# Kernel optimization log

Measured on AMD Instinct MI355X. Metric: run time of the kernel, lower is better.

Reference implementation:

```python
import jax, jax.numpy as jnp
import numpy as np

EPS = 1e-5
AVG_D_LOG = 2.302585092994046  # avg_d['log'] = log(10)

N, D, F, FE = 65536, 16, 64, 16
POST_IN = (4 * 3 + 1) * F  # (n_agg*n_scalers + 1) * in_dim = 832


def setup_inputs() -> dict:
    key = jax.random.key(0)
    ks = jax.random.split(key, 8)
    h = jax.random.normal(ks[0], (N, F), dtype=jnp.float32)
    edge_attr = jax.random.normal(ks[1], (N, D, FE), dtype=jnp.float32)
    nbr_idx = jax.random.randint(ks[2], (N, D), 0, N)
    pre_in = 2 * F + FE
    W_pre = jax.random.normal(ks[3], (pre_in, F), dtype=jnp.float32) / np.sqrt(pre_in)
    b_pre = jnp.zeros((F,), dtype=jnp.float32)
    W_post1 = jax.random.normal(ks[4], (POST_IN, F), dtype=jnp.float32) / np.sqrt(POST_IN)
    b_post1 = jnp.zeros((F,), dtype=jnp.float32)
    W_post2 = jax.random.normal(ks[5], (F, F), dtype=jnp.float32) / np.sqrt(F)
    b_post2 = jnp.zeros((F,), dtype=jnp.float32)
    return {"h": h, "edge_attr": edge_attr, "nbr_idx": nbr_idx,
            "W_pre": W_pre, "b_pre": b_pre,
            "W_post1": W_post1, "b_post1": b_post1,
            "W_post2": W_post2, "b_post2": b_post2}


def reference(h, edge_attr, nbr_idx, W_pre, b_pre, W_post1, b_post1, W_post2, b_post2):
    # pretrans: message MLP on cat([src_feat, dst_feat, edge_attr])
    h_src = h[nbr_idx]                                   # [N, D, F]
    h_dst = jnp.broadcast_to(h[:, None, :], h_src.shape)  # [N, D, F]
    z = jnp.concatenate([h_src, h_dst, edge_attr], axis=-1)  # [N, D, 2F+FE]
    e = jax.nn.relu(jnp.einsum('ndi,io->ndo', z, W_pre) + b_pre)  # [N, D, F]

    # multi-aggregator neighbor reduction (dim=-2)
    mean = jnp.mean(e, axis=-2)
    mx = jnp.max(e, axis=-2)
    mn = jnp.min(e, axis=-2)
    var = jax.nn.relu(jnp.mean(e * e, axis=-2) - mean * mean)
    std = jnp.sqrt(var + EPS)
    agg = jnp.concatenate([mean, mx, mn, std], axis=-1)  # [N, 4F]

    # degree scalers (fixed in-degree D)
    logD = jnp.asarray(np.log(D + 1.0), dtype=h.dtype)
    amp = agg * (logD / AVG_D_LOG)
    att = agg * (AVG_D_LOG / logD)
    agg = jnp.concatenate([agg, amp, att], axis=-1)      # [N, 12F]

    # posttrans MLP on cat([h, aggregated]) with residual (in_dim == out_dim)
    x = jnp.concatenate([h, agg], axis=-1)               # [N, 13F]
    x = jax.nn.relu(x @ W_post1 + b_post1)
    x = x @ W_post2 + b_post2
    return x + h
```

## Files before the change

kernel.cpp:

```cpp
#include <hip/hip_runtime.h>
#include <hip/hip_bf16.h>
#include <math.h>


#define N_NODES 65536
#define NBLK (N_NODES / 16)
#define GRID_PREP (NBLK + 64)
#define ASTRIDE 348
#define YSTRIDE 76

typedef float f32x4 __attribute__((ext_vector_type(4)));
typedef float f32x16 __attribute__((ext_vector_type(16)));
typedef short s16x8 __attribute__((ext_vector_type(8)));
typedef unsigned short us4 __attribute__((ext_vector_type(4)));
typedef int i32x4 __attribute__((ext_vector_type(4)));

__device__ __forceinline__ unsigned short f2bf(float f) {
    union { float f; unsigned int u; } v; v.f = f;
    unsigned int r = v.u + 0x7fffu + ((v.u >> 16) & 1u);
    return (unsigned short)(r >> 16);
}
__device__ __forceinline__ unsigned short f2bfh(float f) {
    __hip_bfloat16 b = __float2bfloat16(f);
    union { __hip_bfloat16 b; unsigned short u; } v; v.b = b; return v.u;
}
__device__ __forceinline__ float bf2f(unsigned short u) {
    union { unsigned int u; float f; } v; v.u = ((unsigned int)u) << 16; return v.f;
}

__global__ __launch_bounds__(256) void k_prep(const float* __restrict__ h,
                                              const float* __restrict__ Wpre,
                                              const float* __restrict__ b_pre,
                                              const float* __restrict__ Wp1,
                                              const float* __restrict__ Wp2,
                                              unsigned short* __restrict__ u,
                                              unsigned short* __restrict__ vbf,
                                              unsigned short* __restrict__ wfullT,
                                              unsigned short* __restrict__ w3T,
                                              unsigned short* __restrict__ wp2T,
                                              float c1, float c2) {
    int t = threadIdx.x;
    if (blockIdx.x >= NBLK) {
        int c = blockIdx.x - NBLK;
        for (int k = t; k < 320; k += 256) {
            float v;
            if (k < 64) v = Wp1[k * 64 + c];
            else {
                int kk = k - 64;
                v = Wp1[(64 + kk) * 64 + c] + c1 * Wp1[(320 + kk) * 64 + c]
                                            + c2 * Wp1[(576 + kk) * 64 + c];
            }
            wfullT[c * 320 + k] = f2bf(v);
        }
        if (t < 16)              w3T[c * 16 + t]         = f2bf(Wpre[(128 + t) * 64 + c]);
        if (t >= 64 && t < 128)  wp2T[c * 64 + (t - 64)] = f2bf(Wp2[(t - 64) * 64 + c]);
        return;
    }

    __shared__ unsigned short hl[16 * 68];
    int lane = t & 63;
    int wv = __builtin_amdgcn_readfirstlane(t) >> 6;
    int c = lane & 15, g = lane >> 4;
    int node0 = blockIdx.x * 16;
    {
        int r = t >> 4, q = t & 15;
        float4 hv = *((const float4*)(h + (size_t)node0 * 64) + t);
        us4 o;
        o.x = f2bfh(hv.x); o.y = f2bfh(hv.y); o.z = f2bfh(hv.z); o.w = f2bfh(hv.w);
        *(us4*)&hl[r * 68 + q * 4] = o;
    }
    s16x8 bf[2][2];
    int woff = (wv < 2) ? 0 : 64;
    #pragma unroll
    for (int i2 = 0; i2 < 2; ++i2) {
        int wcol = ((wv & 1) * 32) + i2 * 16 + c;
        #pragma unroll
        for (int ks = 0; ks < 2; ++ks) {
            #pragma unroll
            for (int j = 0; j < 8; ++j)
                bf[i2][ks][j] = (short)f2bfh(Wpre[(woff + ks * 32 + g * 8 + j) * 64 + wcol]);
        }
    }
    __syncthreads();
    f32x4 acc0 = {0.f, 0.f, 0.f, 0.f}, acc1 = {0.f, 0.f, 0.f, 0.f};
    #pragma unroll
    for (int ks = 0; ks < 2; ++ks) {
        s16x8 a = *(const s16x8*)&hl[c * 68 + ks * 32 + g * 8];
        acc0 = __builtin_amdgcn_mfma_f32_16x16x32_bf16(a, bf[0][ks], acc0, 0, 0, 0);
        acc1 = __builtin_amdgcn_mfma_f32_16x16x32_bf16(a, bf[1][ks], acc1, 0, 0, 0);
    }
    unsigned short* dst = (wv < 2) ? u : vbf;
    #pragma unroll
    for (int i2 = 0; i2 < 2; ++i2) {
        int dcol = ((wv & 1) * 32) + i2 * 16 + c;
        float bp = (wv < 2) ? b_pre[dcol] : 0.f;
        const f32x4& av = i2 ? acc1 : acc0;
        #pragma unroll
        for (int i = 0; i < 4; ++i) {
            int row = g * 4 + i;
            dst[(size_t)(node0 + row) * 64 + dcol] = f2bfh(av[i] + bp);
        }
    }
}

__global__ __launch_bounds__(256, 4) void k_main(
    const float* __restrict__ h,
    const float* __restrict__ edge_attr,
    const int* __restrict__ nbr_idx,
    const float* __restrict__ b_post1,
    const float* __restrict__ b_post2,
    const unsigned short* __restrict__ u,
    const unsigned short* __restrict__ vbf,
    const unsigned short* __restrict__ wfullT,
    const unsigned short* __restrict__ w3T,
    const unsigned short* __restrict__ wp2T,
    float* __restrict__ out) {
    __shared__ unsigned short A_lds[16 * ASTRIDE];
    __shared__ unsigned short y1_lds[16 * YSTRIDE];
    __shared__ int nbl[256];

    int t = threadIdx.x;
    int lane = t & 63;
    int wu2 = __builtin_amdgcn_readfirstlane(t) >> 6;
    int c = lane & 15;
    int g = lane >> 4;
    int l32 = lane & 31;
    int h2 = lane >> 5;
    int ct = wu2 & 1;
    int wr = wu2 >> 1;
    int colb = ct * 32 + l32;
    int cb2 = colb * 2;
    int col16 = wu2 * 16 + c;
    int node0 = blockIdx.x * 16;

    s16x8 w3b = *(const s16x8*)&w3T[colb * 16 + h2 * 8];
    float b1c = b_post1[col16];
    float b2c = b_post2[col16];

    {
        int r = t >> 4, q = t & 15;
        float4 hv = *((const float4*)(h + (size_t)node0 * 64) + t);
        us4 o;
        o.x = f2bfh(hv.x); o.y = f2bfh(hv.y); o.z = f2bfh(hv.z); o.w = f2bfh(hv.w);
        *(us4*)&A_lds[r * ASTRIDE + q * 4] = o;
        nbl[t] = nbr_idx[node0 * 16 + t] << 7;
    }
    __syncthreads();

    const char* ub = (const char*)u;
    const char* vb = (const char*)vbf + ((unsigned)node0 << 7) + (unsigned)(wr * 256) + cb2;
    const char* eb = (const char*)edge_attr
                   + ((size_t)node0 * 16 + wr * 32 + l32) * 64 + h2 * 32;

    #pragma unroll
    for (int it = 0; it < 4; ++it) {
        int rt = wr + 2 * it;

        float4 x0 = *(const float4*)(eb + it * 4096);
        float4 x1 = *(const float4*)(eb + it * 4096 + 16);
        s16x8 a;
        a[0] = (short)f2bfh(x0.x); a[1] = (short)f2bfh(x0.y);
        a[2] = (short)f2bfh(x0.z); a[3] = (short)f2bfh(x0.w);
        a[4] = (short)f2bfh(x1.x); a[5] = (short)f2bfh(x1.y);
        a[6] = (short)f2bfh(x1.z); a[7] = (short)f2bfh(x1.w);

        f32x16 acc = {};
        acc = __builtin_amdgcn_mfma_f32_32x32x16_bf16(a, w3b, acc, 0, 0, 0);

        i32x4 jq0 = *(const i32x4*)&nbl[rt * 32 + 4 * h2 + 0];
        i32x4 jq1 = *(const i32x4*)&nbl[rt * 32 + 4 * h2 + 8];
        i32x4 jq2 = *(const i32x4*)&nbl[rt * 32 + 4 * h2 + 16];
        i32x4 jq3 = *(const i32x4*)&nbl[rt * 32 + 4 * h2 + 24];
        float uv[16];
        #pragma unroll
        for (int i = 0; i < 4; ++i) {
            uv[i]      = bf2f(*(const unsigned short*)(ub + (unsigned)(jq0[i] + cb2)));
            uv[4 + i]  = bf2f(*(const unsigned short*)(ub + (unsigned)(jq1[i] + cb2)));
            uv[8 + i]  = bf2f(*(const unsigned short*)(ub + (unsigned)(jq2[i] + cb2)));
            uv[12 + i] = bf2f(*(const unsigned short*)(ub + (unsigned)(jq3[i] + cb2)));
        }
        float v0 = bf2f(*(const unsigned short*)(vb + it * 512));
        float v1 = bf2f(*(const unsigned short*)(vb + it * 512 + 128));

        float e0  = fmaxf(acc[0]  + uv[0]  + v0, 0.f);
        float e1  = fmaxf(acc[1]  + uv[1]  + v0, 0.f);
        float e2  = fmaxf(acc[2]  + uv[2]  + v0, 0.f);
        float e3  = fmaxf(acc[3]  + uv[3]  + v0, 0.f);
        float e4  = fmaxf(acc[4]  + uv[4]  + v0, 0.f);
        float e5  = fmaxf(acc[5]  + uv[5]  + v0, 0.f);
        float e6  = fmaxf(acc[6]  + uv[6]  + v0, 0.f);
        float e7  = fmaxf(acc[7]  + uv[7]  + v0, 0.f);
        float e8  = fmaxf(acc[8]  + uv[8]  + v1, 0.f);
        float e9  = fmaxf(acc[9]  + uv[9]  + v1, 0.f);
        float e10 = fmaxf(acc[10] + uv[10] + v1, 0.f);
        float e11 = fmaxf(acc[11] + uv[11] + v1, 0.f);
        float e12 = fmaxf(acc[12] + uv[12] + v1, 0.f);
        float e13 = fmaxf(acc[13] + uv[13] + v1, 0.f);
        float e14 = fmaxf(acc[14] + uv[14] + v1, 0.f);
        float e15 = fmaxf(acc[15] + uv[15] + v1, 0.f);

        float s1a = ((e0 + e1) + (e2 + e3)) + ((e4 + e5) + (e6 + e7));
        float s2a = fmaf(e0, e0, fmaf(e1, e1, fmaf(e2, e2, e3 * e3)))
                  + fmaf(e4, e4, fmaf(e5, e5, fmaf(e6, e6, e7 * e7)));
        float mxa = fmaxf(fmaxf(fmaxf(fmaxf(fmaxf(fmaxf(fmaxf(e0, e1), e2), e3), e4), e5), e6), e7);
        float mna = fminf(fminf(fminf(fminf(fminf(fminf(fminf(e0, e1), e2), e3), e4), e5), e6), e7);
        float s1b = ((e8 + e9) + (e10 + e11)) + ((e12 + e13) + (e14 + e15));
        float s2b = fmaf(e8, e8, fmaf(e9, e9, fmaf(e10, e10, e11 * e11)))
                  + fmaf(e12, e12, fmaf(e13, e13, fmaf(e14, e14, e15 * e15)));
        float mxb = fmaxf(fmaxf(fmaxf(fmaxf(fmaxf(fmaxf(fmaxf(e8, e9), e10), e11), e12), e13), e14), e15);
        float mnb = fminf(fminf(fminf(fminf(fminf(fminf(fminf(e8, e9), e10), e11), e12), e13), e14), e15);

        s1a += __shfl_xor(s1a, 32); s2a += __shfl_xor(s2a, 32);
        mxa = fmaxf(mxa, __shfl_xor(mxa, 32)); mna = fminf(mna, __shfl_xor(mna, 32));
        s1b += __shfl_xor(s1b, 32); s2b += __shfl_xor(s2b, 32);
        mxb = fmaxf(mxb, __shfl_xor(mxb, 32)); mnb = fminf(mnb, __shfl_xor(mnb, 32));

        float ma = s1a * 0.0625f;
        float sda = sqrtf(fmaxf(fmaf(-ma, ma, s2a * 0.0625f), 0.f) + 1e-5f);
        float mb = s1b * 0.0625f;
        float sdb = sqrtf(fmaxf(fmaf(-mb, mb, s2b * 0.0625f), 0.f) + 1e-5f);

        if (h2 == 0) {
            unsigned short* pa = &A_lds[(2 * rt) * ASTRIDE + 64 + colb];
            pa[0]   = f2bfh(ma);
            pa[64]  = f2bfh(mxa);
            pa[128] = f2bfh(mna);
            pa[192] = f2bfh(sda);
            unsigned short* pb = &A_lds[(2 * rt + 1) * ASTRIDE + 64 + colb];
            pb[0]   = f2bfh(mb);
            pb[64]  = f2bfh(mxb);
            pb[128] = f2bfh(mnb);
            pb[192] = f2bfh(sdb);
        }
    }
    __syncthreads();

    {
        f32x4 y1 = {0.f, 0.f, 0.f, 0.f};
        #pragma unroll
        for (int ks = 0; ks < 10; ++ks) {
            s16x8 wf = *(const s16x8*)&wfullT[col16 * 320 + ks * 32 + g * 8];
            s16x8 a  = *(const s16x8*)&A_lds[c * ASTRIDE + ks * 32 + g * 8];
            y1 = __builtin_amdgcn_mfma_f32_16x16x32_bf16(a, wf, y1, 0, 0, 0);
        }
        #pragma unroll
        for (int i = 0; i < 4; ++i)
            y1_lds[(g * 4 + i) * YSTRIDE + col16] = f2bfh(fmaxf(y1[i] + b1c, 0.f));
    }
    __syncthreads();

    {
        f32x4 o = {0.f, 0.f, 0.f, 0.f};
        #pragma unroll
        for (int ks = 0; ks < 2; ++ks) {
            s16x8 wf = *(const s16x8*)&wp2T[col16 * 64 + ks * 32 + g * 8];
            s16x8 a  = *(const s16x8*)&y1_lds[c * YSTRIDE + ks * 32 + g * 8];
            o = __builtin_amdgcn_mfma_f32_16x16x32_bf16(a, wf, o, 0, 0, 0);
        }
        #pragma unroll
        for (int i = 0; i < 4; ++i) {
            int r = g * 4 + i;
            out[(size_t)(node0 + r) * 64 + col16] =
                o[i] + b2c + h[(size_t)(node0 + r) * 64 + col16];
        }
    }
}

extern "C" void kernel_launch(void* const* d_in, const int* in_sizes, int n_in,
                              void* d_out, int out_size, void* d_ws, size_t ws_size,
                              hipStream_t stream) {
    const float* h         = (const float*)d_in[0];
    const float* edge_attr = (const float*)d_in[1];
    const int*   nbr_idx   = (const int*)d_in[2];
    const float* W_pre     = (const float*)d_in[3];
    const float* b_pre     = (const float*)d_in[4];
    const float* W_post1   = (const float*)d_in[5];
    const float* b_post1   = (const float*)d_in[6];
    const float* W_post2   = (const float*)d_in[7];
    const float* b_post2   = (const float*)d_in[8];
    float* out = (float*)d_out;

    size_t need = (size_t)N_NODES * 64 * 2 * 2 + (64 * 320 + 64 * 16 + 64 * 64) * 2;
    if (ws_size < need) return;
    unsigned short* u      = (unsigned short*)d_ws;
    unsigned short* vbf    = u + (size_t)N_NODES * 64;
    unsigned short* wfullT = vbf + (size_t)N_NODES * 64;
    unsigned short* w3T    = wfullT + 64 * 320;
    unsigned short* wp2T   = w3T + 64 * 16;

    double ld = log(16.0 + 1.0);
    const double AVG = 2.302585092994046;
    float c1 = (float)(ld / AVG);
    float c2 = (float)(AVG / ld);

    k_prep<<<GRID_PREP, 256, 0, stream>>>(h, W_pre, b_pre, W_post1, W_post2,
                                          u, vbf, wfullT, w3T, wp2T, c1, c2);
    k_main<<<NBLK, 256, 0, stream>>>(h, edge_attr, nbr_idx, b_post1, b_post2,
                                     u, vbf, wfullT, w3T, wp2T, out);
}
```

Before: 64.31 us.

## Software-pipeline neighbor gathers and prefetch post-MLP weights before barriers

The neighbor-index LDS staging and its barrier are removed, and indices are read directly from global memory. The gather loop is restructured into ISSUE/COMPUTE stages so the loads for the next iteration are in flight while the current one computes. The reduction writes are split by half-wave so no lane sits idle. Weight fragments for both post-MLP matmuls are loaded into registers before the barriers so their latency hides behind synchronisation. In exchange, register pressure rises with two stages of gathered values live at once, which under the occupancy target of 4 may cause spills.

```diff
diff --git a/kernel.cpp b/kernel.cpp
--- a/kernel.cpp
+++ b/kernel.cpp
@@ -117,7 +117,6 @@
     float* __restrict__ out) {
     __shared__ unsigned short A_lds[16 * ASTRIDE];
     __shared__ unsigned short y1_lds[16 * YSTRIDE];
-    __shared__ int nbl[256];
 
     int t = threadIdx.x;
     int lane = t & 63;
@@ -137,125 +136,142 @@
     float b1c = b_post1[col16];
     float b2c = b_post2[col16];
 
+    const char* ub = (const char*)u;
+    const char* vb = (const char*)vbf + ((unsigned)node0 << 7) + (unsigned)(wr * 256) + cb2;
+    const char* eb = (const char*)edge_attr
+                   + ((size_t)node0 * 16 + wr * 32 + l32) * 64 + h2 * 32;
+
     {
         int r = t >> 4, q = t & 15;
         float4 hv = *((const float4*)(h + (size_t)node0 * 64) + t);
         us4 o;
         o.x = f2bfh(hv.x); o.y = f2bfh(hv.y); o.z = f2bfh(hv.z); o.w = f2bfh(hv.w);
         *(us4*)&A_lds[r * ASTRIDE + q * 4] = o;
-        nbl[t] = nbr_idx[node0 * 16 + t] << 7;
-    }
-    __syncthreads();
-
-    const char* ub = (const char*)u;
-    const char* vb = (const char*)vbf + ((unsigned)node0 << 7) + (unsigned)(wr * 256) + cb2;
-    const char* eb = (const char*)edge_attr
-                   + ((size_t)node0 * 16 + wr * 32 + l32) * 64 + h2 * 32;
-
+    }
+
+#define ISSUE(S, IT)                                                           \
+    const int* nb##S = nbr_idx + node0 * 16 + (wr + 2 * (IT)) * 32 + 4 * h2;   \
+    i32x4 ja##S = *(const i32x4*)(nb##S);                                      \
+    i32x4 jb##S = *(const i32x4*)(nb##S + 8);                                  \
+    i32x4 jc##S = *(const i32x4*)(nb##S + 16);                                 \
+    i32x4 jd##S = *(const i32x4*)(nb##S + 24);                                 \
+    float4 xa##S = *(const float4*)(eb + (IT) * 4096);                         \
+    float4 xb##S = *(const float4*)(eb + (IT) * 4096 + 16);                    \
+    unsigned short g0##S  = *(const unsigned short*)(ub + (unsigned)((ja##S[0] << 7) + cb2)); \
+    unsigned short g1##S  = *(const unsigned short*)(ub + (unsigned)((ja##S[1] << 7) + cb2)); \
+    unsigned short g2##S  = *(const unsigned short*)(ub + (unsigned)((ja##S[2] << 7) + cb2)); \
+    unsigned short g3##S  = *(const unsigned short*)(ub + (unsigned)((ja##S[3] << 7) + cb2)); \
+    unsigned short g4##S  = *(const unsigned short*)(ub + (unsigned)((jb##S[0] << 7) + cb2)); \
+    unsigned short g5##S  = *(const unsigned short*)(ub + (unsigned)((jb##S[1] << 7) + cb2)); \
+    unsigned short g6##S  = *(const unsigned short*)(ub + (unsigned)((jb##S[2] << 7) + cb2)); \
+    unsigned short g7##S  = *(const unsigned short*)(ub + (unsigned)((jb##S[3] << 7) + cb2)); \
+    unsigned short g8##S  = *(const unsigned short*)(ub + (unsigned)((jc##S[0] << 7) + cb2)); \
+    unsigned short g9##S  = *(const unsigned short*)(ub + (unsigned)((jc##S[1] << 7) + cb2)); \
+    unsigned short g10##S = *(const unsigned short*)(ub + (unsigned)((jc##S[2] << 7) + cb2)); \
+    unsigned short g11##S = *(const unsigned short*)(ub + (unsigned)((jc##S[3] << 7) + cb2)); \
+    unsigned short g12##S = *(const unsigned short*)(ub + (unsigned)((jd##S[0] << 7) + cb2)); \
+    unsigned short g13##S = *(const unsigned short*)(ub + (unsigned)((jd##S[1] << 7) + cb2)); \
+    unsigned short g14##S = *(const unsigned short*)(ub + (unsigned)((jd##S[2] << 7) + cb2)); \
+    unsigned short g15##S = *(const unsigned short*)(ub + (unsigned)((jd##S[3] << 7) + cb2)); \
+    unsigned short va##S = *(const unsigned short*)(vb + (IT) * 512);          \
+    unsigned short vc##S = *(const unsigned short*)(vb + (IT) * 512 + 128);
+
+#define COMPUTE(S, IT) {                                                       \
+    s16x8 a;                                                                   \
+    a[0] = (short)f2bfh(xa##S.x); a[1] = (short)f2bfh(xa##S.y);                \
+    a[2] = (short)f2bfh(xa##S.z); a[3] = (short)f2bfh(xa##S.w);                \
+    a[4] = (short)f2bfh(xb##S.x); a[5] = (short)f2bfh(xb##S.y);                \
+    a[6] = (short)f2bfh(xb##S.z); a[7] = (short)f2bfh(xb##S.w);                \
+    f32x16 acc = {};                                                           \
+    acc = __builtin_amdgcn_mfma_f32_32x32x16_bf16(a, w3b, acc, 0, 0, 0);       \
+    float v0 = bf2f(va##S), v1 = bf2f(vc##S);                                  \
+    float e0  = fmaxf(acc[0]  + bf2f(g0##S)  + v0, 0.f);                       \
+    float e1  = fmaxf(acc[1]  + bf2f(g1##S)  + v0, 0.f);                       \
+    float e2  = fmaxf(acc[2]  + bf2f(g2##S)  + v0, 0.f);                       \
+    float e3  = fmaxf(acc[3]  + bf2f(g3##S)  + v0, 0.f);                       \
+    float e4  = fmaxf(acc[4]  + bf2f(g4##S)  + v0, 0.f);                       \
+    float e5  = fmaxf(acc[5]  + bf2f(g5##S)  + v0, 0.f);                       \
+    float e6  = fmaxf(acc[6]  + bf2f(g6##S)  + v0, 0.f);                       \
+    float e7  = fmaxf(acc[7]  + bf2f(g7##S)  + v0, 0.f);                       \
+    float e8  = fmaxf(acc[8]  + bf2f(g8##S)  + v1, 0.f);                       \
+    float e9  = fmaxf(acc[9]  + bf2f(g9##S)  + v1, 0.f);                       \
+    float e10 = fmaxf(acc[10] + bf2f(g10##S) + v1, 0.f);                       \
+    float e11 = fmaxf(acc[11] + bf2f(g11##S) + v1, 0.f);                       \
+    float e12 = fmaxf(acc[12] + bf2f(g12##S) + v1, 0.f);                       \
+    float e13 = fmaxf(acc[13] + bf2f(g13##S) + v1, 0.f);                       \
+    float e14 = fmaxf(acc[14] + bf2f(g14##S) + v1, 0.f);                       \
+    float e15 = fmaxf(acc[15] + bf2f(g15##S) + v1, 0.f);                       \
+    float s1a = ((e0 + e1) + (e2 + e3)) + ((e4 + e5) + (e6 + e7));             \
+    float s2a = fmaf(e0, e0, fmaf(e1, e1, fmaf(e2, e2, e3 * e3)))              \
+              + fmaf(e4, e4, fmaf(e5, e5, fmaf(e6, e6, e7 * e7)));             \
+    float mxa = fmaxf(fmaxf(fmaxf(e0, e1), fmaxf(e2, e3)),                     \
+                      fmaxf(fmaxf(e4, e5), fmaxf(e6, e7)));                    \
+    float mna = fminf(fminf(fminf(e0, e1), fminf(e2, e3)),                     \
+                      fminf(fminf(e4, e5), fminf(e6, e7)));                    \
+    float s1b = ((e8 + e9) + (e10 + e11)) + ((e12 + e13) + (e14 + e15));       \
+    float s2b = fmaf(e8, e8, fmaf(e9, e9, fmaf(e10, e10, e11 * e11)))          \
+              + fmaf(e12, e12, fmaf(e13, e13, fmaf(e14, e14, e15 * e15)));     \
+    float mxb = fmaxf(fmaxf(fmaxf(e8, e9), fmaxf(e10, e11)),                   \
+                      fmaxf(fmaxf(e12, e13), fmaxf(e14, e15)));                \
+    float mnb = fminf(fminf(fminf(e8, e9), fminf(e10, e11)),                   \
+                      fminf(fminf(e12, e13), fminf(e14, e15)));                \
+    s1a += __shfl_xor(s1a, 32); s2a += __shfl_xor(s2a, 32);                    \
+    mxa = fmaxf(mxa, __shfl_xor(mxa, 32)); mna = fminf(mna, __shfl_xor(mna, 32)); \
+    s1b += __shfl_xor(s1b, 32); s2b += __shfl_xor(s2b, 32);                    \
+    mxb = fmaxf(mxb, __shfl_xor(mxb, 32)); mnb = fminf(mnb, __shfl_xor(mnb, 32)); \
+    float S1 = h2 ? s1b : s1a;                                                 \
+    float S2 = h2 ? s2b : s2a;                                                 \
+    float MX = h2 ? mxb : mxa;                                                 \
+    float MN = h2 ? mnb : mna;                                                 \
+    float M  = S1 * 0.0625f;                                                   \
+    float SD = sqrtf(fmaxf(fmaf(-M, M, S2 * 0.0625f), 0.f) + 1e-5f);           \
+    unsigned short* pd = &A_lds[(2 * (wr + 2 * (IT)) + h2) * ASTRIDE + 64 + colb]; \
+    pd[0]   = f2bfh(M);                                                        \
+    pd[64]  = f2bfh(MX);                                                       \
+    pd[128] = f2bfh(MN);                                                       \
+    pd[192] = f2bfh(SD);                                                       \
+}
+
+    ISSUE(T0, 0)
+    ISSUE(T1, 1)
+    COMPUTE(T0, 0)
+    ISSUE(T2, 2)
+    COMPUTE(T1, 1)
+    ISSUE(T3, 3)
+    COMPUTE(T2, 2)
+    COMPUTE(T3, 3)
+#undef ISSUE
+#undef COMPUTE
+
+    s16x8 wf[10];
     #pragma unroll
-    for (int it = 0; it < 4; ++it) {
-        int rt = wr + 2 * it;
-
-        float4 x0 = *(const float4*)(eb + it * 4096);
-        float4 x1 = *(const float4*)(eb + it * 4096 + 16);
-        s16x8 a;
-        a[0] = (short)f2bfh(x0.x); a[1] = (short)f2bfh(x0.y);
-        a[2] = (short)f2bfh(x0.z); a[3] = (short)f2bfh(x0.w);
-        a[4] = (short)f2bfh(x1.x); a[5] = (short)f2bfh(x1.y);
-        a[6] = (short)f2bfh(x1.z); a[7] = (short)f2bfh(x1.w);
-
-        f32x16 acc = {};
-        acc = __builtin_amdgcn_mfma_f32_32x32x16_bf16(a, w3b, acc, 0, 0, 0);
-
-        i32x4 jq0 = *(const i32x4*)&nbl[rt * 32 + 4 * h2 + 0];
-        i32x4 jq1 = *(const i32x4*)&nbl[rt * 32 + 4 * h2 + 8];
-        i32x4 jq2 = *(const i32x4*)&nbl[rt * 32 + 4 * h2 + 16];
-        i32x4 jq3 = *(const i32x4*)&nbl[rt * 32 + 4 * h2 + 24];
-        float uv[16];
-        #pragma unroll
-        for (int i = 0; i < 4; ++i) {
-            uv[i]      = bf2f(*(const unsigned short*)(ub + (unsigned)(jq0[i] + cb2)));
-            uv[4 + i]  = bf2f(*(const unsigned short*)(ub + (unsigned)(jq1[i] + cb2)));
-            uv[8 + i]  = bf2f(*(const unsigned short*)(ub + (unsigned)(jq2[i] + cb2)));
-            uv[12 + i] = bf2f(*(const unsigned short*)(ub + (unsigned)(jq3[i] + cb2)));
-        }
-        float v0 = bf2f(*(const unsigned short*)(vb + it * 512));
-        float v1 = bf2f(*(const unsigned short*)(vb + it * 512 + 128));
-
-        float e0  = fmaxf(acc[0]  + uv[0]  + v0, 0.f);
-        float e1  = fmaxf(acc[1]  + uv[1]  + v0, 0.f);
-        float e2  = fmaxf(acc[2]  + uv[2]  + v0, 0.f);
-        float e3  = fmaxf(acc[3]  + uv[3]  + v0, 0.f);
-        float e4  = fmaxf(acc[4]  + uv[4]  + v0, 0.f);
-        float e5  = fmaxf(acc[5]  + uv[5]  + v0, 0.f);
-        float e6  = fmaxf(acc[6]  + uv[6]  + v0, 0.f);
-        float e7  = fmaxf(acc[7]  + uv[7]  + v0, 0.f);
-        float e8  = fmaxf(acc[8]  + uv[8]  + v1, 0.f);
-        float e9  = fmaxf(acc[9]  + uv[9]  + v1, 0.f);
-        float e10 = fmaxf(acc[10] + uv[10] + v1, 0.f);
-        float e11 = fmaxf(acc[11] + uv[11] + v1, 0.f);
-        float e12 = fmaxf(acc[12] + uv[12] + v1, 0.f);
-        float e13 = fmaxf(acc[13] + uv[13] + v1, 0.f);
-        float e14 = fmaxf(acc[14] + uv[14] + v1, 0.f);
-        float e15 = fmaxf(acc[15] + uv[15] + v1, 0.f);
-
-        float s1a = ((e0 + e1) + (e2 + e3)) + ((e4 + e5) + (e6 + e7));
-        float s2a = fmaf(e0, e0, fmaf(e1, e1, fmaf(e2, e2, e3 * e3)))
-                  + fmaf(e4, e4, fmaf(e5, e5, fmaf(e6, e6, e7 * e7)));
-        float mxa = fmaxf(fmaxf(fmaxf(fmaxf(fmaxf(fmaxf(fmaxf(e0, e1), e2), e3), e4), e5), e6), e7);
-        float mna = fminf(fminf(fminf(fminf(fminf(fminf(fminf(e0, e1), e2), e3), e4), e5), e6), e7);
-        float s1b = ((e8 + e9) + (e10 + e11)) + ((e12 + e13) + (e14 + e15));
-        float s2b = fmaf(e8, e8, fmaf(e9, e9, fmaf(e10, e10, e11 * e11)))
-                  + fmaf(e12, e12, fmaf(e13, e13, fmaf(e14, e14, e15 * e15)));
-        float mxb = fmaxf(fmaxf(fmaxf(fmaxf(fmaxf(fmaxf(fmaxf(e8, e9), e10), e11), e12), e13), e14), e15);
-        float mnb = fminf(fminf(fminf(fminf(fminf(fminf(fminf(e8, e9), e10), e11), e12), e13), e14), e15);
-
-        s1a += __shfl_xor(s1a, 32); s2a += __shfl_xor(s2a, 32);
-        mxa = fmaxf(mxa, __shfl_xor(mxa, 32)); mna = fminf(mna, __shfl_xor(mna, 32));
-        s1b += __shfl_xor(s1b, 32); s2b += __shfl_xor(s2b, 32);
-        mxb = fmaxf(mxb, __shfl_xor(mxb, 32)); mnb = fminf(mnb, __shfl_xor(mnb, 32));
-
-        float ma = s1a * 0.0625f;
-        float sda = sqrtf(fmaxf(fmaf(-ma, ma, s2a * 0.0625f), 0.f) + 1e-5f);
-        float mb = s1b * 0.0625f;
-        float sdb = sqrtf(fmaxf(fmaf(-mb, mb, s2b * 0.0625f), 0.f) + 1e-5f);
-
-        if (h2 == 0) {
-            unsigned short* pa = &A_lds[(2 * rt) * ASTRIDE + 64 + colb];
-            pa[0]   = f2bfh(ma);
-            pa[64]  = f2bfh(mxa);
-            pa[128] = f2bfh(mna);
-            pa[192] = f2bfh(sda);
-            unsigned short* pb = &A_lds[(2 * rt + 1) * ASTRIDE + 64 + colb];
-            pb[0]   = f2bfh(mb);
-            pb[64]  = f2bfh(mxb);
-            pb[128] = f2bfh(mnb);
-            pb[192] = f2bfh(sdb);
-        }
-    }
+    for (int ks = 0; ks < 10; ++ks)
+        wf[ks] = *(const s16x8*)&wfullT[col16 * 320 + ks * 32 + g * 8];
     __syncthreads();
 
     {
         f32x4 y1 = {0.f, 0.f, 0.f, 0.f};
         #pragma unroll
         for (int ks = 0; ks < 10; ++ks) {
-            s16x8 wf = *(const s16x8*)&wfullT[col16 * 320 + ks * 32 + g * 8];
-            s16x8 a  = *(const s16x8*)&A_lds[c * ASTRIDE + ks * 32 + g * 8];
-            y1 = __builtin_amdgcn_mfma_f32_16x16x32_bf16(a, wf, y1, 0, 0, 0);
+            s16x8 a = *(const s16x8*)&A_lds[c * ASTRIDE + ks * 32 + g * 8];
+            y1 = __builtin_amdgcn_mfma_f32_16x16x32_bf16(a, wf[ks], y1, 0, 0, 0);
         }
         #pragma unroll
         for (int i = 0; i < 4; ++i)
             y1_lds[(g * 4 + i) * YSTRIDE + col16] = f2bfh(fmaxf(y1[i] + b1c, 0.f));
     }
+
+    s16x8 wp0 = *(const s16x8*)&wp2T[col16 * 64 + 0 * 32 + g * 8];
+    s16x8 wp1 = *(const s16x8*)&wp2T[col16 * 64 + 1 * 32 + g * 8];
     __syncthreads();
 
     {
         f32x4 o = {0.f, 0.f, 0.f, 0.f};
-        #pragma unroll
-        for (int ks = 0; ks < 2; ++ks) {
-            s16x8 wf = *(const s16x8*)&wp2T[col16 * 64 + ks * 32 + g * 8];
-            s16x8 a  = *(const s16x8*)&y1_lds[c * YSTRIDE + ks * 32 + g * 8];
-            o = __builtin_amdgcn_mfma_f32_16x16x32_bf16(a, wf, o, 0, 0, 0);
+        {
+            s16x8 a0 = *(const s16x8*)&y1_lds[c * YSTRIDE + 0 * 32 + g * 8];
+            s16x8 a1 = *(const s16x8*)&y1_lds[c * YSTRIDE + 1 * 32 + g * 8];
+            o = __builtin_amdgcn_mfma_f32_16x16x32_bf16(a0, wp0, o, 0, 0, 0);
+            o = __builtin_amdgcn_mfma_f32_16x16x32_bf16(a1, wp1, o, 0, 0, 0);
         }
         #pragma unroll
         for (int i = 0; i < 4; ++i) {
```

After: 66.19 us. +2.9%, slower.
